# Performance work log

Measured on AMD Instinct MI355X. Metric: run time of the kernel, lower is better.

Reference implementation:

```python
import jax, jax.numpy as jnp
import numpy as np

NUM_LAYERS = 4
INPUT_SIZE = 1024
RNN_SIZE = 1024
BATCH = 128


def setup_inputs() -> dict:
    key = jax.random.key(0)
    ks = jax.random.split(key, 7)
    H4 = 4 * RNN_SIZE
    return {
        "x": jax.random.normal(ks[0], (BATCH, INPUT_SIZE), dtype=jnp.float32),
        "h0": jax.random.normal(ks[1], (NUM_LAYERS, BATCH, RNN_SIZE), dtype=jnp.float32),
        "c0": jax.random.normal(ks[2], (NUM_LAYERS, BATCH, RNN_SIZE), dtype=jnp.float32),
        "W_ih": jax.random.normal(ks[3], (NUM_LAYERS, H4, INPUT_SIZE), dtype=jnp.float32) * 0.02,
        "W_hh": jax.random.normal(ks[4], (NUM_LAYERS, H4, RNN_SIZE), dtype=jnp.float32) * 0.02,
        "b_ih": jax.random.normal(ks[5], (NUM_LAYERS, H4), dtype=jnp.float32) * 0.02,
        "b_hh": jax.random.normal(ks[6], (NUM_LAYERS, H4), dtype=jnp.float32) * 0.02,
    }


def _lstm_cell(x, h, c, w_ih, w_hh, bi, bh):
    # gates: [B, 4H], PyTorch LSTMCell order (i, f, g, o)
    gates = x @ w_ih.T + bi + h @ w_hh.T + bh
    i, f, g, o = jnp.split(gates, 4, axis=-1)
    i = jax.nn.sigmoid(i)
    f = jax.nn.sigmoid(f)
    g = jnp.tanh(g)
    o = jax.nn.sigmoid(o)
    c1 = f * c + i * g
    h1 = o * jnp.tanh(c1)
    return h1, c1


def reference(x, h0, c0, W_ih, W_hh, b_ih, b_hh):
    # Stacked single-timestep LSTM with input feeding (dropout=0.0 -> identity).
    inp = x
    h1s, c1s = [], []
    for i in range(NUM_LAYERS):
        h1, c1 = _lstm_cell(inp, h0[i], c0[i], W_ih[i], W_hh[i], b_ih[i], b_hh[i])
        inp = h1  # dropout(p=0) is identity between layers
        h1s.append(h1)
        c1s.append(c1)
    return inp, jnp.stack(h1s), jnp.stack(c1s)
```

## Files before the change

### kernel.cpp

```cpp
#include <hip/hip_runtime.h>

#define NLAYER 4
#define B_ 128
#define D_ 1024
#define H4_ 4096
#define K_ 2048
#define BK 64
#define NCH 32
#define OUTSEC 131072

typedef float f32x4 __attribute__((ext_vector_type(4)));
typedef _Float16 h8 __attribute__((ext_vector_type(8)));
typedef _Float16 h4 __attribute__((ext_vector_type(4)));

#define LDS_AH 0
#define LDS_WH 32768
#define LDS_WL 36864
#define LDS_TOT 40960

__device__ __forceinline__ void stage16(const void* gsrc, char* lds_uniform, int lane) {
#if __has_builtin(__builtin_amdgcn_global_load_lds)
  __builtin_amdgcn_global_load_lds((const __attribute__((address_space(1))) void*)gsrc,
                                   (__attribute__((address_space(3))) void*)lds_uniform,
                                   16, 0, 0);
#else
  *(h8*)(lds_uniform + lane * 16) = *(const h8*)gsrc;
#endif
}

struct ALF { h8 v[4]; };

__global__ __launch_bounds__(256)
void prep_kernel(const float* __restrict__ x, const float* __restrict__ h0,
                 _Float16* __restrict__ Ah, _Float16* __restrict__ Al)
{
  int i = (blockIdx.x * 256 + threadIdx.x) * 4;
  const float* src;
  int dst;
  if (i < 131072) {
    int b = i >> 10, k = i & 1023;
    src = x + i;
    dst = b * K_ + k;
  } else {
    int j = i - 131072;
    int l = j >> 17, r = j & 131071;
    int b = r >> 10, k = r & 1023;
    src = h0 + j;
    dst = l * (B_ * K_) + b * K_ + D_ + k;
  }
  f32x4 v = *(const f32x4*)src;
  h4 hi, lo;
#pragma unroll
  for (int j2 = 0; j2 < 4; ++j2) {
    _Float16 h = (_Float16)v[j2];
    hi[j2] = h;
    lo[j2] = (_Float16)((v[j2] - (float)h) * 4096.0f);
  }
  *(h4*)(Ah + dst) = hi;
  *(h4*)(Al + dst) = lo;
}

__global__ __launch_bounds__(256)
void lstm_layer(const float* __restrict__ Wih, const float* __restrict__ Whh,
                const float* __restrict__ bih, const float* __restrict__ bhh,
                const float* __restrict__ c0,
                const _Float16* __restrict__ Ah, const _Float16* __restrict__ Al,
                _Float16* __restrict__ AhN, _Float16* __restrict__ AlN,
                float* __restrict__ out, int layer)
{
  __shared__ __align__(16) char smem[LDS_TOT];
  const int tid  = threadIdx.x;
  const int lane = tid & 63;
  const int wid  = tid >> 6;
  const int u0   = blockIdx.x * 4;

  const int wrow = tid >> 4;
  const int kq   = tid & 15;
  const int wr   = (wrow & 3) * D_ + u0 + (wrow >> 2);
  const float* wih_p = Wih + (size_t)wr * D_ + kq * 4;
  const float* whh_p = Whh + (size_t)wr * D_ + kq * 4;
  const int wbyte = wrow * 128 + ((kq * 8) ^ ((wrow & 7) << 4));

  const int R0   = wid * 32 + (lane >> 3);
  const int cswz = ((lane & 7) ^ (lane >> 3)) * 8;
  const _Float16* ahg = Ah + (size_t)R0 * K_ + cswz;

  const int arow = wid * 32 + (lane & 15);
  const int aswz = (lane & 7) << 4;
  const int wn = lane & 15, wc = lane >> 4;
  const int wswz = (wn & 7) << 4;
  const _Float16* alg = Al + (size_t)arow * K_ + wc * 8;

  f32x4 acc_h[2] = {{0.f,0.f,0.f,0.f},{0.f,0.f,0.f,0.f}};
  f32x4 acc_s[2] = {{0.f,0.f,0.f,0.f},{0.f,0.f,0.f,0.f}};

  auto loadW = [&](int t) -> f32x4 {
    const float* p = (t < 16) ? (wih_p + t * BK) : (whh_p + (t - 16) * BK);
    return *(const f32x4*)p;
  };
  auto stageA = [&](int t, int buf) {
    const _Float16* g = ahg + t * BK;
    char* lb = smem + LDS_AH + buf * 16384 + wid * 4096;
    stage16(g,            lb,        lane);
    stage16(g +  8 * K_,  lb + 1024, lane);
    stage16(g + 16 * K_,  lb + 2048, lane);
    stage16(g + 24 * K_,  lb + 3072, lane);
  };
  auto stageW = [&](f32x4 w, int buf) {
    h4 hi, lo;
#pragma unroll
    for (int j = 0; j < 4; ++j) {
      _Float16 h = (_Float16)w[j];
      hi[j] = h;
      lo[j] = (_Float16)((w[j] - (float)h) * 4096.0f);
    }
    *(h4*)(smem + LDS_WH + buf * 2048 + wbyte) = hi;
    *(h4*)(smem + LDS_WL + buf * 2048 + wbyte) = lo;
  };
  auto loadAL = [&](int t) -> ALF {
    ALF r;
#pragma unroll
    for (int m = 0; m < 2; ++m)
#pragma unroll
      for (int ks = 0; ks < 2; ++ks)
        r.v[m * 2 + ks] = *(const h8*)(alg + (size_t)m * 16 * K_ + t * BK + ks * 32);
    return r;
  };
  auto mfmaChunk = [&](int buf, const ALF& alf) {
    const char* ab  = smem + LDS_AH + buf * 16384;
    const char* whb = smem + LDS_WH + buf * 2048;
    const char* wlb = smem + LDS_WL + buf * 2048;
    h8 a[2][2], wh[2], wl[2];
#pragma unroll
    for (int ks = 0; ks < 2; ++ks) {
      int wo = wn * 128 + ((ks * 64 + wc * 16) ^ wswz);
      wh[ks] = *(const h8*)(whb + wo);
      wl[ks] = *(const h8*)(wlb + wo);
#pragma unroll
      for (int m = 0; m < 2; ++m)
        a[m][ks] = *(const h8*)(ab + (arow + m * 16) * 128 + ((ks * 64 + wc * 16) ^ aswz));
    }
#pragma unroll
    for (int m = 0; m < 2; ++m)
#pragma unroll
      for (int ks = 0; ks < 2; ++ks) {
        acc_h[m] = __builtin_amdgcn_mfma_f32_16x16x32_f16(a[m][ks],        wh[ks], acc_h[m], 0, 0, 0);
        acc_s[m] = __builtin_amdgcn_mfma_f32_16x16x32_f16(alf.v[m*2+ks],   wh[ks], acc_s[m], 0, 0, 0);
        acc_s[m] = __builtin_amdgcn_mfma_f32_16x16x32_f16(a[m][ks],        wl[ks], acc_s[m], 0, 0, 0);
      }
  };

  f32x4 w0  = loadW(0);
  f32x4 wnB = loadW(1);
  f32x4 wnA = loadW(2);
  ALF alfA = loadAL(0);
  ALF alfB;
  stageA(0, 0);
  stageW(w0, 0);
  __syncthreads();

  for (int t = 0; t < NCH; t += 2) {
    stageA(t + 1, 1);
    alfB = loadAL(t + 1);
    mfmaChunk(0, alfA);
    stageW(wnB, 1);
    if (t + 3 < NCH) wnB = loadW(t + 3);
    __syncthreads();
    if (t + 2 < NCH) { stageA(t + 2, 0); alfA = loadAL(t + 2); }
    mfmaChunk(1, alfB);
    if (t + 2 < NCH) stageW(wnA, 0);
    if (t + 4 < NCH) wnA = loadW(t + 4);
    __syncthreads();
  }

  float* cb   = (float*)smem;
  float* mycb = cb + wid * 528;
  const float INV = 1.0f / 4096.0f;
#pragma unroll
  for (int m = 0; m < 2; ++m)
#pragma unroll
    for (int j = 0; j < 4; ++j) {
      int r32 = m * 16 + (lane >> 4) * 4 + j;
      mycb[(lane & 15) * 33 + r32] = acc_h[m][j] + acc_s[m][j] * INV;
    }
  __syncthreads();

#pragma unroll
  for (int it = 0; it < 2; ++it) {
    int cid = it * 64 + lane;
    int du = cid >> 5, r32 = cid & 31;
    int row = wid * 32 + r32;
    int u = u0 + du;
    float gi = mycb[(du * 4 + 0) * 33 + r32] + bih[u]           + bhh[u];
    float gf = mycb[(du * 4 + 1) * 33 + r32] + bih[D_ + u]      + bhh[D_ + u];
    float gg = mycb[(du * 4 + 2) * 33 + r32] + bih[2 * D_ + u]  + bhh[2 * D_ + u];
    float go = mycb[(du * 4 + 3) * 33 + r32] + bih[3 * D_ + u]  + bhh[3 * D_ + u];
    float iv = 1.0f / (1.0f + __expf(-gi));
    float fv = 1.0f / (1.0f + __expf(-gf));
    float gv = tanhf(gg);
    float ov = 1.0f / (1.0f + __expf(-go));
    float c0v = c0[row * D_ + u];
    float c1  = fv * c0v + iv * gv;
    float h1v = ov * tanhf(c1);
    out[(5 + layer) * OUTSEC + row * D_ + u] = c1;
    out[(1 + layer) * OUTSEC + row * D_ + u] = h1v;
    if (layer == 3) {
      out[row * D_ + u] = h1v;
    } else {
      _Float16 hh = (_Float16)h1v;
      AhN[row * K_ + u] = hh;
      AlN[row * K_ + u] = (_Float16)((h1v - (float)hh) * 4096.0f);
    }
  }
}

extern "C" void kernel_launch(void* const* d_in, const int* in_sizes, int n_in,
                              void* d_out, int out_size, void* d_ws, size_t ws_size,
                              hipStream_t stream)
{
  const float* x   = (const float*)d_in[0];
  const float* h0  = (const float*)d_in[1];
  const float* c0  = (const float*)d_in[2];
  const float* Wih = (const float*)d_in[3];
  const float* Whh = (const float*)d_in[4];
  const float* bih = (const float*)d_in[5];
  const float* bhh = (const float*)d_in[6];
  float* out = (float*)d_out;

  _Float16* Ah = (_Float16*)d_ws;
  _Float16* Al = Ah + 4 * B_ * K_;

  prep_kernel<<<640, 256, 0, stream>>>(x, h0, Ah, Al);
  for (int l = 0; l < NLAYER; ++l) {
    lstm_layer<<<256, 256, 0, stream>>>(
        Wih + (size_t)l * H4_ * D_, Whh + (size_t)l * H4_ * D_,
        bih + l * H4_, bhh + l * H4_,
        c0 + l * (B_ * D_),
        Ah + l * (B_ * K_), Al + l * (B_ * K_),
        (l < 3) ? Ah + (l + 1) * (B_ * K_) : (_Float16*)nullptr,
        (l < 3) ? Al + (l + 1) * (B_ * K_) : (_Float16*)nullptr,
        out, l);
  }
}
```

Baseline: 273.5 us.

## Split-K the per-layer LSTM GEMM into four partials and a separate cell kernel

Each layer's fused GEMM+cell kernel becomes a split-K GEMM over 1024 blocks: each block covers a quarter of the 2048-long K dimension and writes fp32 partial gates to workspace. A separate elementwise kernel sums the four partials, adds a combined bias precomputed in the prep kernel, and applies the LSTM cell. Weight hi/lo fp16 splitting now happens directly in registers instead of being staged through LDS. The goal is more parallelism and occupancy for a weight-bandwidth-bound GEMM, paid for with extra partial-sum traffic and twice as many kernel launches per layer.

```diff
diff --git a/kernel.cpp b/kernel.cpp
--- a/kernel.cpp
+++ b/kernel.cpp
@@ -5,18 +5,16 @@
 #define D_ 1024
 #define H4_ 4096
 #define K_ 2048
-#define BK 64
-#define NCH 32
 #define OUTSEC 131072
+#define CH_PER 8
+#define GP_STRIDE 524288
 
 typedef float f32x4 __attribute__((ext_vector_type(4)));
 typedef _Float16 h8 __attribute__((ext_vector_type(8)));
 typedef _Float16 h4 __attribute__((ext_vector_type(4)));
 
-#define LDS_AH 0
-#define LDS_WH 32768
-#define LDS_WL 36864
-#define LDS_TOT 40960
+struct ALF { h8 v[4]; };
+struct W4  { f32x4 a, b, c, d; };
 
 __device__ __forceinline__ void stage16(const void* gsrc, char* lds_uniform, int lane) {
 #if __has_builtin(__builtin_amdgcn_global_load_lds)
@@ -28,12 +26,22 @@
 #endif
 }
 
-struct ALF { h8 v[4]; };
-
 __global__ __launch_bounds__(256)
 void prep_kernel(const float* __restrict__ x, const float* __restrict__ h0,
-                 _Float16* __restrict__ Ah, _Float16* __restrict__ Al)
-{
+                 const float* __restrict__ bih, const float* __restrict__ bhh,
+                 _Float16* __restrict__ Ah, _Float16* __restrict__ Al,
+                 float* __restrict__ b4)
+{
+  if (blockIdx.x >= 640) {
+    int idx = (blockIdx.x - 640) * 256 + threadIdx.x;
+    int l = idx >> 10, u = idx & 1023;
+    f32x4 r;
+#pragma unroll
+    for (int q = 0; q < 4; ++q)
+      r[q] = bih[l * H4_ + q * D_ + u] + bhh[l * H4_ + q * D_ + u];
+    *(f32x4*)(b4 + (size_t)idx * 4) = r;
+    return;
+  }
   int i = (blockIdx.x * 256 + threadIdx.x) * 4;
   const float* src;
   int dst;
@@ -60,157 +68,155 @@
   *(h4*)(Al + dst) = lo;
 }
 
-__global__ __launch_bounds__(256)
-void lstm_layer(const float* __restrict__ Wih, const float* __restrict__ Whh,
-                const float* __restrict__ bih, const float* __restrict__ bhh,
-                const float* __restrict__ c0,
-                const _Float16* __restrict__ Ah, const _Float16* __restrict__ Al,
-                _Float16* __restrict__ AhN, _Float16* __restrict__ AlN,
-                float* __restrict__ out, int layer)
-{
-  __shared__ __align__(16) char smem[LDS_TOT];
+__global__ __launch_bounds__(256, 4)
+void gemm_part(const float* __restrict__ Wih, const float* __restrict__ Whh,
+               const _Float16* __restrict__ Ah, const _Float16* __restrict__ Al,
+               float* __restrict__ gp)
+{
+  __shared__ __align__(16) char smem[32768];
   const int tid  = threadIdx.x;
   const int lane = tid & 63;
   const int wid  = tid >> 6;
-  const int u0   = blockIdx.x * 4;
-
-  const int wrow = tid >> 4;
-  const int kq   = tid & 15;
-  const int wr   = (wrow & 3) * D_ + u0 + (wrow >> 2);
-  const float* wih_p = Wih + (size_t)wr * D_ + kq * 4;
-  const float* whh_p = Whh + (size_t)wr * D_ + kq * 4;
-  const int wbyte = wrow * 128 + ((kq * 8) ^ ((wrow & 7) << 4));
+  const int bidx = blockIdx.x;
+  const int s    = bidx & 3;
+  const int nt   = bidx >> 2;
+  const int u0   = nt * 4;
+  const int k0   = s * 512;
+
+  const int n16 = lane & 15;
+  const int kq  = lane >> 4;
+  const int wr  = ((n16 & 3) << 10) + u0 + (n16 >> 2);
+  const float* wbase = (s < 2) ? (Wih + k0) : (Whh + (k0 - 1024));
+  const float* wp = wbase + (size_t)wr * D_ + kq * 8;
 
   const int R0   = wid * 32 + (lane >> 3);
   const int cswz = ((lane & 7) ^ (lane >> 3)) * 8;
-  const _Float16* ahg = Ah + (size_t)R0 * K_ + cswz;
-
-  const int arow = wid * 32 + (lane & 15);
+  const _Float16* ahg = Ah + (size_t)R0 * K_ + k0 + cswz;
+
+  const int arow = wid * 32 + n16;
   const int aswz = (lane & 7) << 4;
-  const int wn = lane & 15, wc = lane >> 4;
-  const int wswz = (wn & 7) << 4;
-  const _Float16* alg = Al + (size_t)arow * K_ + wc * 8;
+  const _Float16* alg = Al + (size_t)arow * K_ + k0 + kq * 8;
 
   f32x4 acc_h[2] = {{0.f,0.f,0.f,0.f},{0.f,0.f,0.f,0.f}};
   f32x4 acc_s[2] = {{0.f,0.f,0.f,0.f},{0.f,0.f,0.f,0.f}};
 
-  auto loadW = [&](int t) -> f32x4 {
-    const float* p = (t < 16) ? (wih_p + t * BK) : (whh_p + (t - 16) * BK);
-    return *(const f32x4*)p;
+  auto loadW = [&](int t) -> W4 {
+    const float* p = wp + t * 64;
+    W4 r;
+    r.a = *(const f32x4*)(p);
+    r.b = *(const f32x4*)(p + 4);
+    r.c = *(const f32x4*)(p + 32);
+    r.d = *(const f32x4*)(p + 36);
+    return r;
   };
   auto stageA = [&](int t, int buf) {
-    const _Float16* g = ahg + t * BK;
-    char* lb = smem + LDS_AH + buf * 16384 + wid * 4096;
+    const _Float16* g = ahg + t * 64;
+    char* lb = smem + buf * 16384 + wid * 4096;
     stage16(g,            lb,        lane);
     stage16(g +  8 * K_,  lb + 1024, lane);
     stage16(g + 16 * K_,  lb + 2048, lane);
     stage16(g + 24 * K_,  lb + 3072, lane);
   };
-  auto stageW = [&](f32x4 w, int buf) {
-    h4 hi, lo;
-#pragma unroll
-    for (int j = 0; j < 4; ++j) {
-      _Float16 h = (_Float16)w[j];
-      hi[j] = h;
-      lo[j] = (_Float16)((w[j] - (float)h) * 4096.0f);
-    }
-    *(h4*)(smem + LDS_WH + buf * 2048 + wbyte) = hi;
-    *(h4*)(smem + LDS_WL + buf * 2048 + wbyte) = lo;
-  };
   auto loadAL = [&](int t) -> ALF {
     ALF r;
 #pragma unroll
     for (int m = 0; m < 2; ++m)
 #pragma unroll
       for (int ks = 0; ks < 2; ++ks)
-        r.v[m * 2 + ks] = *(const h8*)(alg + (size_t)m * 16 * K_ + t * BK + ks * 32);
+        r.v[m * 2 + ks] = *(const h8*)(alg + (size_t)m * 16 * K_ + t * 64 + ks * 32);
     return r;
   };
-  auto mfmaChunk = [&](int buf, const ALF& alf) {
-    const char* ab  = smem + LDS_AH + buf * 16384;
-    const char* whb = smem + LDS_WH + buf * 2048;
-    const char* wlb = smem + LDS_WL + buf * 2048;
-    h8 a[2][2], wh[2], wl[2];
-#pragma unroll
-    for (int ks = 0; ks < 2; ++ks) {
-      int wo = wn * 128 + ((ks * 64 + wc * 16) ^ wswz);
-      wh[ks] = *(const h8*)(whb + wo);
-      wl[ks] = *(const h8*)(wlb + wo);
+
+  W4  wreg = loadW(0);
+  ALF alf[2];
+  alf[0] = loadAL(0);
+  stageA(0, 0);
+  __syncthreads();
+
+#pragma unroll
+  for (int t = 0; t < CH_PER; ++t) {
+    h8 whi[2], wlo[2];
+    {
+      const f32x4* wv = &wreg.a;
+#pragma unroll
+      for (int ks = 0; ks < 2; ++ks)
+#pragma unroll
+        for (int j = 0; j < 8; ++j) {
+          float f = wv[ks * 2 + (j >> 2)][j & 3];
+          _Float16 h = (_Float16)f;
+          whi[ks][j] = h;
+          wlo[ks][j] = (_Float16)((f - (float)h) * 4096.0f);
+        }
+    }
+    if (t + 1 < CH_PER) {
+      stageA(t + 1, (t + 1) & 1);
+      alf[(t + 1) & 1] = loadAL(t + 1);
+      wreg = loadW(t + 1);
+    }
+    {
+      const char* ab = smem + (t & 1) * 16384;
+      h8 a[2][2];
+#pragma unroll
+      for (int ks = 0; ks < 2; ++ks)
+#pragma unroll
+        for (int m = 0; m < 2; ++m)
+          a[m][ks] = *(const h8*)(ab + (arow + m * 16) * 128 + ((ks * 64 + kq * 16) ^ aswz));
 #pragma unroll
       for (int m = 0; m < 2; ++m)
-        a[m][ks] = *(const h8*)(ab + (arow + m * 16) * 128 + ((ks * 64 + wc * 16) ^ aswz));
-    }
-#pragma unroll
-    for (int m = 0; m < 2; ++m)
-#pragma unroll
-      for (int ks = 0; ks < 2; ++ks) {
-        acc_h[m] = __builtin_amdgcn_mfma_f32_16x16x32_f16(a[m][ks],        wh[ks], acc_h[m], 0, 0, 0);
-        acc_s[m] = __builtin_amdgcn_mfma_f32_16x16x32_f16(alf.v[m*2+ks],   wh[ks], acc_s[m], 0, 0, 0);
-        acc_s[m] = __builtin_amdgcn_mfma_f32_16x16x32_f16(a[m][ks],        wl[ks], acc_s[m], 0, 0, 0);
-      }
-  };
-
-  f32x4 w0  = loadW(0);
-  f32x4 wnB = loadW(1);
-  f32x4 wnA = loadW(2);
-  ALF alfA = loadAL(0);
-  ALF alfB;
-  stageA(0, 0);
-  stageW(w0, 0);
-  __syncthreads();
-
-  for (int t = 0; t < NCH; t += 2) {
-    stageA(t + 1, 1);
-    alfB = loadAL(t + 1);
-    mfmaChunk(0, alfA);
-    stageW(wnB, 1);
-    if (t + 3 < NCH) wnB = loadW(t + 3);
+#pragma unroll
+        for (int ks = 0; ks < 2; ++ks) {
+          acc_h[m] = __builtin_amdgcn_mfma_f32_16x16x32_f16(a[m][ks],             whi[ks], acc_h[m], 0, 0, 0);
+          acc_s[m] = __builtin_amdgcn_mfma_f32_16x16x32_f16(alf[t & 1].v[m*2+ks], whi[ks], acc_s[m], 0, 0, 0);
+          acc_s[m] = __builtin_amdgcn_mfma_f32_16x16x32_f16(a[m][ks],             wlo[ks], acc_s[m], 0, 0, 0);
+        }
+    }
     __syncthreads();
-    if (t + 2 < NCH) { stageA(t + 2, 0); alfA = loadAL(t + 2); }
-    mfmaChunk(1, alfB);
-    if (t + 2 < NCH) stageW(wnA, 0);
-    if (t + 4 < NCH) wnA = loadW(t + 4);
-    __syncthreads();
-  }
-
-  float* cb   = (float*)smem;
-  float* mycb = cb + wid * 528;
+  }
+
   const float INV = 1.0f / 4096.0f;
+  float* gout = gp + (size_t)s * GP_STRIDE + (size_t)(nt * 16 + n16);
 #pragma unroll
   for (int m = 0; m < 2; ++m)
 #pragma unroll
     for (int j = 0; j < 4; ++j) {
-      int r32 = m * 16 + (lane >> 4) * 4 + j;
-      mycb[(lane & 15) * 33 + r32] = acc_h[m][j] + acc_s[m][j] * INV;
-    }
-  __syncthreads();
-
-#pragma unroll
-  for (int it = 0; it < 2; ++it) {
-    int cid = it * 64 + lane;
-    int du = cid >> 5, r32 = cid & 31;
-    int row = wid * 32 + r32;
-    int u = u0 + du;
-    float gi = mycb[(du * 4 + 0) * 33 + r32] + bih[u]           + bhh[u];
-    float gf = mycb[(du * 4 + 1) * 33 + r32] + bih[D_ + u]      + bhh[D_ + u];
-    float gg = mycb[(du * 4 + 2) * 33 + r32] + bih[2 * D_ + u]  + bhh[2 * D_ + u];
-    float go = mycb[(du * 4 + 3) * 33 + r32] + bih[3 * D_ + u]  + bhh[3 * D_ + u];
-    float iv = 1.0f / (1.0f + __expf(-gi));
-    float fv = 1.0f / (1.0f + __expf(-gf));
-    float gv = tanhf(gg);
-    float ov = 1.0f / (1.0f + __expf(-go));
-    float c0v = c0[row * D_ + u];
-    float c1  = fv * c0v + iv * gv;
-    float h1v = ov * tanhf(c1);
-    out[(5 + layer) * OUTSEC + row * D_ + u] = c1;
-    out[(1 + layer) * OUTSEC + row * D_ + u] = h1v;
-    if (layer == 3) {
-      out[row * D_ + u] = h1v;
-    } else {
-      _Float16 hh = (_Float16)h1v;
-      AhN[row * K_ + u] = hh;
-      AlN[row * K_ + u] = (_Float16)((h1v - (float)hh) * 4096.0f);
-    }
+      int row = wid * 32 + m * 16 + kq * 4 + j;
+      gout[(size_t)row * H4_] = acc_h[m][j] + acc_s[m][j] * INV;
+    }
+}
+
+__global__ __launch_bounds__(256)
+void cell_kernel(const float* __restrict__ gp, const float* __restrict__ b4,
+                 const float* __restrict__ c0, float* __restrict__ out,
+                 _Float16* __restrict__ AhN, _Float16* __restrict__ AlN, int layer)
+{
+  int i = blockIdx.x * 256 + threadIdx.x;
+  int row = i >> 10, u = i & 1023;
+  int c4 = ((u >> 2) << 4) + ((u & 3) << 2);
+  const float* g0 = gp + (size_t)row * H4_ + c4;
+  f32x4 g = *(const f32x4*)(g0);
+  g += *(const f32x4*)(g0 + GP_STRIDE);
+  g += *(const f32x4*)(g0 + 2 * (size_t)GP_STRIDE);
+  g += *(const f32x4*)(g0 + 3 * (size_t)GP_STRIDE);
+  f32x4 bb = *(const f32x4*)(b4 + (size_t)u * 4);
+  float gi = g[0] + bb[0];
+  float gf = g[1] + bb[1];
+  float gg = g[2] + bb[2];
+  float go = g[3] + bb[3];
+  float iv = 1.0f / (1.0f + __expf(-gi));
+  float fv = 1.0f / (1.0f + __expf(-gf));
+  float gv = tanhf(gg);
+  float ov = 1.0f / (1.0f + __expf(-go));
+  float c0v = c0[i];
+  float c1  = fv * c0v + iv * gv;
+  float h1v = ov * tanhf(c1);
+  out[(5 + layer) * OUTSEC + i] = c1;
+  out[(1 + layer) * OUTSEC + i] = h1v;
+  if (layer == 3) {
+    out[i] = h1v;
+  } else {
+    _Float16 hh = (_Float16)h1v;
+    AhN[(size_t)row * K_ + u] = hh;
+    AlN[(size_t)row * K_ + u] = (_Float16)((h1v - (float)hh) * 4096.0f);
   }
 }
 
@@ -229,16 +235,17 @@
 
   _Float16* Ah = (_Float16*)d_ws;
   _Float16* Al = Ah + 4 * B_ * K_;
-
-  prep_kernel<<<640, 256, 0, stream>>>(x, h0, Ah, Al);
+  float* gp = (float*)((char*)d_ws + 4u * 1024 * 1024);
+  float* b4 = (float*)((char*)d_ws + 12u * 1024 * 1024);
+
+  prep_kernel<<<656, 256, 0, stream>>>(x, h0, bih, bhh, Ah, Al, b4);
   for (int l = 0; l < NLAYER; ++l) {
-    lstm_layer<<<256, 256, 0, stream>>>(
+    gemm_part<<<1024, 256, 0, stream>>>(
         Wih + (size_t)l * H4_ * D_, Whh + (size_t)l * H4_ * D_,
-        bih + l * H4_, bhh + l * H4_,
-        c0 + l * (B_ * D_),
-        Ah + l * (B_ * K_), Al + l * (B_ * K_),
-        (l < 3) ? Ah + (l + 1) * (B_ * K_) : (_Float16*)nullptr,
-        (l < 3) ? Al + (l + 1) * (B_ * K_) : (_Float16*)nullptr,
-        out, l);
-  }
-}
+        Ah + (size_t)l * B_ * K_, Al + (size_t)l * B_ * K_, gp);
+    cell_kernel<<<512, 256, 0, stream>>>(
+        gp, b4 + (size_t)l * 4096, c0 + (size_t)l * OUTSEC, out,
+        (l < 3) ? Ah + (size_t)(l + 1) * B_ * K_ : (_Float16*)nullptr,
+        (l < 3) ? Al + (size_t)(l + 1) * B_ * K_ : (_Float16*)nullptr, l);
+  }
+}
```

After: 302.0 us. 1.1x slower.
